# Performance work log

Measured on AMD Instinct MI355X. Metric: run time of the kernel, lower is better.

The kernel has to match this reference:

```python
import jax, jax.numpy as jnp
import numpy as np

DIM = 256
NH = 8
HGT = 32
WID = 32
B = 8


def rel_indices(S):
    # (1, S*S, S*S, 3) with channels (dx, dy, d^2), matching torch construction
    ind = jnp.arange(S)[None, :] - jnp.arange(S)[:, None]          # (S,S)
    indx = jnp.tile(ind, (S, S))                                    # (S^2,S^2)
    indy = jnp.repeat(jnp.repeat(ind, S, axis=0), S, axis=1)        # (S^2,S^2)
    indd = indx ** 2 + indy ** 2
    return jnp.stack([indx, indy, indd], axis=-1).astype(jnp.float32)[None]


def setup_inputs() -> dict:
    key = jax.random.key(0)
    ks = jax.random.split(key, 8)
    std = 0.02
    x = jax.random.normal(ks[0], (B, DIM, HGT, WID), dtype=jnp.float32)
    input_mask = jnp.ones((B, HGT, WID), dtype=jnp.float32)
    Wqk = jax.random.normal(ks[1], (2 * DIM, DIM), dtype=jnp.float32) * std  # qkv_bias=False
    Wv = jax.random.normal(ks[2], (DIM, DIM), dtype=jnp.float32) * std
    Wproj = jax.random.normal(ks[3], (DIM, DIM), dtype=jnp.float32) * std
    bproj = jnp.zeros((DIM,), dtype=jnp.float32)
    Wpos = jax.random.normal(ks[4], (NH, 3), dtype=jnp.float32) * std
    bpos = jnp.zeros((NH,), dtype=jnp.float32)
    gating = jnp.ones((NH,), dtype=jnp.float32)
    return {"x": x, "input_mask": input_mask, "Wqk": Wqk, "Wv": Wv,
            "Wproj": Wproj, "bproj": bproj, "Wpos": Wpos, "bpos": bpos,
            "gating": gating}


def gpsa_forward(x, input_mask, Wqk, Wv, Wproj, bproj, Wpos, bpos, gating):
    Bq, C, H, W = x.shape
    N = H * W
    nh = gating.shape[0]
    hd = C // nh
    scale = hd ** (-0.5)

    xf = x.reshape(Bq, C, N).transpose(0, 2, 1)          # (B,N,C)
    m = input_mask.reshape(Bq, N)                        # (B,N)

    qk = (xf @ Wqk.T).reshape(Bq, N, 2, nh, hd)
    q = qk[:, :, 0].transpose(0, 2, 1, 3)                # (B,nh,N,hd)
    k = qk[:, :, 1].transpose(0, 2, 1, 3)

    patch_score = jax.nn.softmax(
        jnp.einsum('bhnd,bhmd->bhnm', q, k) * scale, axis=-1)

    rel = rel_indices(H)                                  # (1,N,N,3)
    pos_score = jnp.einsum('unmt,ht->uhnm', rel, Wpos) + bpos[None, :, None, None]
    pos_score = jax.nn.softmax(pos_score, axis=-1)        # (1,nh,N,N)

    g = jax.nn.sigmoid(gating)[None, :, None, None]
    attn = (1.0 - g) * patch_score + g * pos_score
    attn = attn / attn.sum(axis=-1, keepdims=True)
    attn = attn * m[:, None, None, :]                     # mask keys
    attn = attn / attn.sum(axis=-1, keepdims=True)

    v = (xf @ Wv.T).reshape(Bq, N, nh, hd).transpose(0, 2, 1, 3)  # (B,nh,N,hd)
    out = jnp.einsum('bhnm,bhmd->bhnd', attn, v)          # (B,nh,N,hd)
    out = out.transpose(0, 2, 1, 3).reshape(Bq, N, C)
    out = out @ Wproj.T + bproj
    return out.transpose(0, 2, 1).reshape(Bq, C, H, W)


def reference(x, input_mask, Wqk, Wv, Wproj, bproj, Wpos, bpos, gating):
    return gpsa_forward(x, input_mask, Wqk, Wv, Wproj, bproj, Wpos, bpos, gating)
```

## Files before the change

kernel.cpp:

```cpp
#include <hip/hip_runtime.h>
#include <hip/hip_bf16.h>
#include <math.h>

#define B_ 8
#define C_ 256
#define N_ 1024
#define NH_ 8
#define HD_ 32

typedef __attribute__((ext_vector_type(8))) short bf16x8;
typedef __attribute__((ext_vector_type(4))) short bf16x4;
typedef __attribute__((ext_vector_type(4))) float f32x4;
typedef __attribute__((ext_vector_type(16))) float f32x16;
typedef __attribute__((ext_vector_type(2))) unsigned int u32x2;
typedef __attribute__((ext_vector_type(4))) unsigned int u32x4;
#define MFMA16(a,b,c) __builtin_amdgcn_mfma_f32_16x16x32_bf16((a),(b),(c),0,0,0)
#define MFMA32(a,b,c) __builtin_amdgcn_mfma_f32_32x32x16_bf16((a),(b),(c),0,0,0)

static __device__ __forceinline__ short f2bf(float f) {
    __hip_bfloat16 h = __float2bfloat16(f);
    return *reinterpret_cast<short*>(&h);
}
static __device__ __forceinline__ unsigned int cvtpk(float a, float b) {
    unsigned int r;
    asm("v_cvt_pk_bf16_f32 %0, %1, %2" : "=v"(r) : "v"(a), "v"(b));
    return r;
}

#define FS 0.2550352584f

static constexpr size_t OFF_VB   = 0;
static constexpr size_t OFF_QBF  = 8388608;
static constexpr size_t OFF_KFR  = 12582912;
static constexpr size_t OFF_VFR  = 16777216;
static constexpr size_t OFF_E1   = 20971520;
static constexpr size_t OFF_E2   = 21004288;
static constexpr size_t OFF_SE1  = 21037056;
static constexpr size_t OFF_SE2  = 21038080;
static constexpr size_t OFF_A2   = 21039104;
static constexpr size_t A2S      = 36;
static constexpr size_t OFF_O    = 30476288;
static constexpr size_t OFF_WBF  = 34670592;
static constexpr size_t OFF_WPBF = 35063808;
static constexpr size_t OFF_ZFR  = 35194880;

__global__ __launch_bounds__(256) void k_prep(
    const float* __restrict__ Wqk, const float* __restrict__ Wv,
    const float* __restrict__ Wp, const float* __restrict__ mask,
    const float* __restrict__ Wpos, const float* __restrict__ bpos,
    __hip_bfloat16* __restrict__ wfm, __hip_bfloat16* __restrict__ wpfm,
    __hip_bfloat16* __restrict__ zfrag,
    float* __restrict__ e1, float* __restrict__ e2,
    float* __restrict__ se1, float* __restrict__ se2)
{
    const int bx = blockIdx.x;
    const int tid = threadIdx.x;
    __shared__ float ps[2][32][8];
    if (bx < 256) {
        int idx = bx * 256 + tid;
        int row = idx >> 6;
        int c4  = (idx & 63) * 4;
        const float* src = (row < 512) ? (Wqk + (size_t)row*256)
                         : (row < 768) ? (Wv + (size_t)(row-512)*256)
                                       : (Wp + (size_t)(row-768)*256);
        float4 v = *(const float4*)(src + c4);
        bf16x4 pk;
        pk[0] = f2bf(v.x); pk[1] = f2bf(v.y); pk[2] = f2bf(v.z); pk[3] = f2bf(v.w);
        int r2 = (row < 768) ? row : (row - 768);
        __hip_bfloat16* dst = (row < 768) ? wfm : wpfm;
        size_t addr = (size_t)(r2 >> 4)*4096 + (size_t)(c4 >> 5)*512
                    + (size_t)((((c4 >> 3) & 3)*16) + (r2 & 15))*8 + (c4 & 7);
        *(bf16x4*)(dst + addr) = pk;
    } else if (bx < 384) {
        int idx = (bx - 256) * 256 + tid;
        int L8  = idx & 127;
        int mt  = (idx >> 7) & 31;
        int b   = idx >> 12;
        int region = L8 >> 6;
        int slot   = L8 & 63;
        int zrow = slot & 31, shi = slot >> 5;
        bf16x8 v;
        if (zrow == 0) {
            int m = mt*32 + region*16 + shi*8;
            const float* mp = mask + (size_t)b*N_ + m;
            #pragma unroll
            for (int j = 0; j < 8; ++j) v[j] = f2bf(mp[j]);
        } else {
            short c = (zrow == 1) ? (short)0x3F80 : (short)0;
            #pragma unroll
            for (int j = 0; j < 8; ++j) v[j] = c;
        }
        *(bf16x8*)(zfrag + ((size_t)b*32 + mt)*1024 + region*512 + slot*8) = v;
    } else {
        const int h = bx - 384;
        const int i = tid >> 3, j4 = (tid & 7) * 4;
        const float wx = Wpos[h*3+0], wy = Wpos[h*3+1], wd = Wpos[h*3+2], bp = bpos[h];
        float fmx = -1e30f, gmx = -1e30f;
        for (int jp = 0; jp < 32; ++jp) {
            float dx = (float)(jp - i);
            float q2 = wd*dx*dx;
            fmx = fmaxf(fmx, wx*dx + q2 + bp);
            gmx = fmaxf(gmx, wy*dx + q2);
        }
        float s1 = 0.f, s2 = 0.f;
        #pragma unroll
        for (int jj = 0; jj < 4; ++jj) {
            int j = j4 + jj;
            float dx = (float)(j - i);
            float q2 = wd*dx*dx;
            float fv = __expf(wx*dx + q2 + bp - fmx);
            float gv = __expf(wy*dx + q2 - gmx);
            e1[h*1024 + i*32 + j] = fv;
            e2[h*1024 + i*32 + j] = gv;
            s1 += fv; s2 += gv;
        }
        ps[0][i][tid & 7] = s1;
        ps[1][i][tid & 7] = s2;
        __syncthreads();
        if (tid < 32) {
            float a = 0.f, c = 0.f;
            #pragma unroll
            for (int k = 0; k < 8; ++k) { a += ps[0][tid][k]; c += ps[1][tid][k]; }
            se1[h*32 + tid] = a;
            se2[h*32 + tid] = c;
        }
    }
}

__global__ __launch_bounds__(256) void k_xT(
    const float* __restrict__ x, __hip_bfloat16* __restrict__ xfm)
{
    const int n0 = blockIdx.x * 64, c0 = blockIdx.y * 64, b = blockIdx.z;
    __shared__ float tile[64][68];
    const int t = threadIdx.x;
    {
        int cl = t >> 2, nq = (t & 3) * 16;
        const float* src = x + ((size_t)b*C_ + c0 + cl)*N_ + n0 + nq;
        #pragma unroll
        for (int i = 0; i < 4; ++i)
            *(float4*)&tile[cl][nq + i*4] = ((const float4*)src)[i];
    }
    __syncthreads();
    {
        int nl = t >> 2, cq = (t & 3) * 16;
        short pk[16];
        #pragma unroll
        for (int i = 0; i < 16; ++i) pk[i] = f2bf(tile[cq + i][nl]);
        int cg = c0 + cq;
        int ks = cg >> 5, g0 = (cg >> 3) & 3;
        size_t base = ((size_t)b*64 + (n0 >> 4) + (nl >> 4))*4096
                    + (size_t)ks*512 + (size_t)(g0*16 + (nl & 15))*8;
        *(uint4*)(xfm + base)       = *(uint4*)&pk[0];
        *(uint4*)(xfm + base + 128) = *(uint4*)&pk[8];
    }
}

__global__ __launch_bounds__(256) void k_qkv_mfma(
    const __hip_bfloat16* __restrict__ xfm, const __hip_bfloat16* __restrict__ wfm,
    const float* __restrict__ mask,
    __hip_bfloat16* __restrict__ qbf, __hip_bfloat16* __restrict__ kfrag,
    __hip_bfloat16* __restrict__ vfrag, float* __restrict__ vbuf)
{
    const int t = threadIdx.x, w = t >> 6, L = t & 63, lo = L & 15, g = L >> 4;
    const int jw = blockIdx.x * 64 + w * 16;
    const int n0 = blockIdx.y * 64, b = blockIdx.z;

    const __hip_bfloat16* afm = wfm + (size_t)(jw >> 4)*4096 + (size_t)L*8;
    bf16x8 af[8];
    #pragma unroll
    for (int ks = 0; ks < 8; ++ks) af[ks] = *(const bf16x8*)(afm + ks*512);

    const f32x4 Z = {0.f,0.f,0.f,0.f};
    f32x4 D0 = Z, D1 = Z, D2 = Z, D3 = Z;
    const __hip_bfloat16* xb = xfm + ((size_t)b*64 + (n0 >> 4))*4096 + (size_t)L*8;
    #pragma unroll
    for (int ks = 0; ks < 8; ++ks) {
        bf16x8 b0 = *(const bf16x8*)(xb + ks*512);
        bf16x8 b1 = *(const bf16x8*)(xb + 4096 + ks*512);
        bf16x8 b2 = *(const bf16x8*)(xb + 8192 + ks*512);
        bf16x8 b3 = *(const bf16x8*)(xb + 12288 + ks*512);
        D0 = MFMA16(af[ks], b0, D0);
        D1 = MFMA16(af[ks], b1, D1);
        D2 = MFMA16(af[ks], b2, D2);
        D3 = MFMA16(af[ks], b3, D3);
    }
    f32x4 D[4] = {D0, D1, D2, D3};

    const size_t bb = (size_t)b*NH_;
    if (jw < 256) {
        int h = jw >> 5, d0 = (jw & 31) + 4*g;
        #pragma unroll
        for (int nt = 0; nt < 4; ++nt) {
            int nn = n0 + nt*16 + lo;
            bf16x4 pk;
            #pragma unroll
            for (int r = 0; r < 4; ++r) pk[r] = f2bf(D[nt][r] * FS);
            *(bf16x4*)(qbf + ((bb + h)*N_ + nn)*HD_ + d0) = pk;
        }
    } else if (jw < 512) {
        int j2 = jw & 255, h = j2 >> 5, d0 = (j2 & 31) + 4*g;
        size_t base = (bb + h)*32768 + (size_t)(d0 >> 4)*512
                    + (size_t)((d0 >> 3) & 1)*256 + (d0 & 7);
        #pragma unroll
        for (int nt = 0; nt < 4; ++nt) {
            int nn = n0 + nt*16 + lo;
            bf16x4 pk;
            #pragma unroll
            for (int r = 0; r < 4; ++r) pk[r] = f2bf(D[nt][r]);
            *(bf16x4*)(kfrag + base + (size_t)(nn >> 5)*1024 + (nn & 31)*8) = pk;
        }
    } else {
        int j2 = jw - 512, h = j2 >> 5, d0 = (j2 & 31) + 4*g;
        #pragma unroll
        for (int nt = 0; nt < 4; ++nt) {
            int nn = n0 + nt*16 + lo;
            float mval = mask[(size_t)b*N_ + nn];
            float4 fv = make_float4(D[nt][0], D[nt][1], D[nt][2], D[nt][3]);
            *(float4*)(vbuf + ((bb + h)*N_ + nn)*HD_ + d0) = fv;
            size_t vbase = (bb + h)*32768 + (size_t)(nn >> 5)*1024
                         + (size_t)((nn >> 4) & 1)*512 + (size_t)((nn >> 3) & 1)*256
                         + (nn & 7);
            #pragma unroll
            for (int r = 0; r < 4; ++r)
                vfrag[vbase + (size_t)(d0 + r)*8] = __float2bfloat16(D[nt][r] * mval);
        }
    }
}

__global__ __launch_bounds__(256) void k_pos_apply(
    const float* __restrict__ vb, const float* __restrict__ mask,
    const float* __restrict__ e1, const float* __restrict__ e2,
    float* __restrict__ a2)
{
    const int rn = blockIdx.x, h = blockIdx.y, b = blockIdx.z;
    const int tid = threadIdx.x;
    const int cm = tid >> 3, dq = tid & 7;
    __shared__ float t1[32][36];
    __shared__ float e1s[32][36];
    __shared__ float t1m[32];
    __shared__ float e2s[32];
    const float* vbh = vb + (((size_t)b*NH_ + h)*N_)*HD_;
    const float* mb  = mask + (size_t)b*N_;

    {
        int r = tid >> 3, c4 = (tid & 7) * 4;
        *(float4*)&e1s[r][c4] = *(const float4*)(e1 + h*1024 + r*32 + c4);
        if (tid < 32) e2s[tid] = e2[h*1024 + rn*32 + tid];
    }
    __syncthreads();

    {
        float4 acc = make_float4(0.f,0.f,0.f,0.f);
        const float* vcol = vbh + cm*HD_ + dq*4;
        #pragma unroll 8
        for (int rm = 0; rm < 32; ++rm) {
            float4 vv = *(const float4*)(vcol + (size_t)rm*32*HD_);
            float wgt = e2s[rm];
            acc.x = fmaf(wgt, vv.x, acc.x);
            acc.y = fmaf(wgt, vv.y, acc.y);
            acc.z = fmaf(wgt, vv.z, acc.z);
            acc.w = fmaf(wgt, vv.w, acc.w);
        }
        *(float4*)&t1[cm][dq*4] = acc;
    }
    if (tid < 32) {
        float s = 0.f;
        for (int rm = 0; rm < 32; ++rm)
            s = fmaf(e2s[rm], mb[rm*32 + tid], s);
        t1m[tid] = s;
    }
    __syncthreads();

    const size_t bh = (size_t)b*NH_ + h;
    {
        const int cn = cm;
        float4 acc = make_float4(0.f,0.f,0.f,0.f);
        #pragma unroll 8
        for (int ci = 0; ci < 32; ++ci) {
            float wgt = e1s[cn][ci];
            float4 tv = *(const float4*)&t1[ci][dq*4];
            acc.x = fmaf(wgt, tv.x, acc.x);
            acc.y = fmaf(wgt, tv.y, acc.y);
            acc.z = fmaf(wgt, tv.z, acc.z);
            acc.w = fmaf(wgt, tv.w, acc.w);
        }
        int n = rn*32 + cn;
        *(float4*)(a2 + (bh*N_ + n)*A2S + dq*4) = acc;
    }
    if (tid < 32) {
        float s = 0.f;
        for (int ci = 0; ci < 32; ++ci)
            s = fmaf(e1s[tid][ci], t1m[ci], s);
        a2[(bh*N_ + rn*32 + tid)*A2S + 32] = s;
    }
}

__global__ __launch_bounds__(512, 4) void k_attn_mfma(
    const __hip_bfloat16* __restrict__ qbf, const __hip_bfloat16* __restrict__ kfrag,
    const __hip_bfloat16* __restrict__ vfrag, const __hip_bfloat16* __restrict__ zfrag,
    const float* __restrict__ a2, const float* __restrict__ se1,
    const float* __restrict__ se2, const float* __restrict__ gating,
    __hip_bfloat16* __restrict__ ob)
{
    const int bid = blockIdx.x;
    const int swz = ((bid & 7) << 6) | (bid >> 3);
    const int xt = swz & 7, h = (swz >> 3) & 7, b = swz >> 6;

    const int t = threadIdx.x, w = t >> 6, L = t & 63;
    const int ln = L & 31, hi = L >> 5;
    const int nh = w & 3, sp = w >> 2;
    const int n0 = xt * 128 + nh * 32;
    const size_t bh = (size_t)b*NH_ + h;
    const __hip_bfloat16* qh = qbf + bh*(size_t)N_*HD_;
    const size_t spo = (size_t)sp * 16 * 1024;
    const __hip_bfloat16* kf = kfrag + bh*32768 + spo + (size_t)L*8;
    const __hip_bfloat16* vf = vfrag + bh*32768 + spo + (size_t)L*8;
    const __hip_bfloat16* zf = zfrag + (size_t)b*32768 + spo + (size_t)L*8;

    __shared__ float ldsO[128*32];
    __shared__ float ldsZ[128*2];

    bf16x8 qf0 = *(const bf16x8*)(qh + (size_t)(n0 + ln)*HD_ + 8*hi);
    bf16x8 qf1 = *(const bf16x8*)(qh + (size_t)(n0 + ln)*HD_ + 16 + 8*hi);

    f32x16 O; f32x16 Zc;
    #pragma unroll
    for (int i = 0; i < 16; ++i) { O[i] = 0.f; Zc[i] = 0.f; }

    bf16x8 ka0 = *(const bf16x8*)(kf);
    bf16x8 ka1 = *(const bf16x8*)(kf + 512);
    bf16x8 vf0 = *(const bf16x8*)(vf);
    bf16x8 vf1 = *(const bf16x8*)(vf + 512);
    bf16x8 zf0 = *(const bf16x8*)(zf);
    bf16x8 zf1 = *(const bf16x8*)(zf + 512);

    for (int mt = 0; mt < 16; ++mt) {
        f32x16 S;
        #pragma unroll
        for (int i = 0; i < 16; ++i) S[i] = 0.f;
        S = MFMA32(ka0, qf0, S);
        S = MFMA32(ka1, qf1, S);

        const size_t o1 = (size_t)(mt < 15 ? mt + 1 : mt) * 1024;
        bf16x8 nka0 = *(const bf16x8*)(kf + o1);
        bf16x8 nka1 = *(const bf16x8*)(kf + o1 + 512);
        bf16x8 nvf0 = *(const bf16x8*)(vf + o1);
        bf16x8 nvf1 = *(const bf16x8*)(vf + o1 + 512);
        bf16x8 nzf0 = *(const bf16x8*)(zf + o1);
        bf16x8 nzf1 = *(const bf16x8*)(zf + o1 + 512);

        float e[16];
        #pragma unroll
        for (int i = 0; i < 16; ++i) e[i] = exp2f(S[i]);

        unsigned int x01 = cvtpk(e[0], e[1]), x23 = cvtpk(e[2], e[3]);
        unsigned int x45 = cvtpk(e[4], e[5]), x67 = cvtpk(e[6], e[7]);
        u32x2 r02 = __builtin_amdgcn_permlane32_swap(x01, x45, false, false);
        u32x2 r13 = __builtin_amdgcn_permlane32_swap(x23, x67, false, false);
        u32x4 p0u = { r02[0], r13[0], r02[1], r13[1] };
        bf16x8 pa0 = *reinterpret_cast<bf16x8*>(&p0u);
        unsigned int y01 = cvtpk(e[8], e[9]),  y23 = cvtpk(e[10], e[11]);
        unsigned int y45 = cvtpk(e[12], e[13]), y67 = cvtpk(e[14], e[15]);
        u32x2 s02 = __builtin_amdgcn_permlane32_swap(y01, y45, false, false);
        u32x2 s13 = __builtin_amdgcn_permlane32_swap(y23, y67, false, false);
        u32x4 p1u = { s02[0], s13[0], s02[1], s13[1] };
        bf16x8 pa1 = *reinterpret_cast<bf16x8*>(&p1u);

        O  = MFMA32(pa0, vf0, O);
        O  = MFMA32(pa1, vf1, O);
        Zc = MFMA32(pa0, zf0, Zc);
        Zc = MFMA32(pa1, zf1, Zc);

        ka0 = nka0; ka1 = nka1; vf0 = nvf0; vf1 = nvf1; zf0 = nzf0; zf1 = nzf1;
    }

    if (sp == 1) {
        #pragma unroll
        for (int r = 0; r < 16; ++r) {
            int nl = nh*32 + (r&3) + 8*(r>>2) + 4*hi;
            ldsO[nl*32 + ln] = O[r];
        }
        if (ln < 2) {
            #pragma unroll
            for (int r = 0; r < 16; ++r) {
                int nl = nh*32 + (r&3) + 8*(r>>2) + 4*hi;
                ldsZ[nl*2 + ln] = Zc[r];
            }
        }
    }
    __syncthreads();
    if (sp == 0) {
        #pragma unroll
        for (int r = 0; r < 16; ++r) {
            int nl = nh*32 + (r&3) + 8*(r>>2) + 4*hi;
            O[r] += ldsO[nl*32 + ln];
            if (ln < 2) Zc[r] += ldsZ[nl*2 + ln];
        }

        const float gs = 1.f / (1.f + __expf(-gating[h]));
        #pragma unroll
        for (int r = 0; r < 16; ++r) {
            const int n = n0 + (r&3) + 8*(r>>2) + 4*hi;
            float z1m = __shfl(Zc[r], (L & 32) | 0);
            float zsv = __shfl(Zc[r], (L & 32) | 1);
            const float* a2p = a2 + (bh*N_ + n)*A2S;
            float z2m = a2p[32];
            float zp  = se1[h*32 + (n & 31)] * se2[h*32 + (n >> 5)];
            float w1  = (1.f - gs) / zsv;
            float w2  = gs / zp;
            float inv = 1.f / (w1*z1m + w2*z2m);
            float o = (w1*O[r] + w2*a2p[ln]) * inv;
            ob[((size_t)b*N_ + n)*C_ + h*HD_ + ln] = __float2bfloat16(o);
        }
    }
}

__global__ __launch_bounds__(256) void k_proj_mfma(
    const __hip_bfloat16* __restrict__ obf, const __hip_bfloat16* __restrict__ wpfm,
    const float* __restrict__ bp, float* __restrict__ out)
{
    const int t = threadIdx.x, w = t >> 6, L = t & 63, lo = L & 15, g = L >> 4;
    const int cw = blockIdx.x * 64 + w * 16;
    const int n0 = blockIdx.y * 64, b = blockIdx.z;

    const __hip_bfloat16* afm = wpfm + (size_t)(cw >> 4)*4096 + (size_t)L*8;
    bf16x8 af[8];
    #pragma unroll
    for (int ks = 0; ks < 8; ++ks) af[ks] = *(const bf16x8*)(afm + ks*512);

    const f32x4 Z = {0.f,0.f,0.f,0.f};
    f32x4 D0 = Z, D1 = Z, D2 = Z, D3 = Z;
    const __hip_bfloat16* xb = obf + ((size_t)b*N_ + n0 + lo)*256 + 8*g;
    #pragma unroll
    for (int ks = 0; ks < 8; ++ks) {
        bf16x8 b0 = *(const bf16x8*)(xb + ks*32);
        bf16x8 b1 = *(const bf16x8*)(xb + 16*256 + ks*32);
        bf16x8 b2 = *(const bf16x8*)(xb + 32*256 + ks*32);
        bf16x8 b3 = *(const bf16x8*)(xb + 48*256 + ks*32);
        D0 = MFMA16(af[ks], b0, D0);
        D1 = MFMA16(af[ks], b1, D1);
        D2 = MFMA16(af[ks], b2, D2);
        D3 = MFMA16(af[ks], b3, D3);
    }
    f32x4 D[4] = {D0, D1, D2, D3};

    float bias[4];
    #pragma unroll
    for (int r = 0; r < 4; ++r) bias[r] = bp[cw + 4*g + r];
    #pragma unroll
    for (int nt = 0; nt < 4; ++nt) {
        int nn = n0 + nt*16 + lo;
        #pragma unroll
        for (int r = 0; r < 4; ++r)
            out[((size_t)b*C_ + cw + 4*g + r)*N_ + nn] = D[nt][r] + bias[r];
    }
}

extern "C" void kernel_launch(void* const* d_in, const int* in_sizes, int n_in,
                              void* d_out, int out_size, void* d_ws, size_t ws_size,
                              hipStream_t stream)
{
    (void)in_sizes; (void)n_in; (void)out_size; (void)ws_size;
    const float* x      = (const float*)d_in[0];
    const float* mask   = (const float*)d_in[1];
    const float* Wqk    = (const float*)d_in[2];
    const float* Wv     = (const float*)d_in[3];
    const float* Wproj  = (const float*)d_in[4];
    const float* bproj  = (const float*)d_in[5];
    const float* Wpos   = (const float*)d_in[6];
    const float* bpos   = (const float*)d_in[7];
    const float* gating = (const float*)d_in[8];
    float* out = (float*)d_out;
    char* w = (char*)d_ws;

    float*          vbuf  = (float*)(w + OFF_VB);
    __hip_bfloat16* qbf   = (__hip_bfloat16*)(w + OFF_QBF);
    __hip_bfloat16* kfrag = (__hip_bfloat16*)(w + OFF_KFR);
    __hip_bfloat16* vfrag = (__hip_bfloat16*)(w + OFF_VFR);
    float*          e1    = (float*)(w + OFF_E1);
    float*          e2    = (float*)(w + OFF_E2);
    float*          se1   = (float*)(w + OFF_SE1);
    float*          se2   = (float*)(w + OFF_SE2);
    float*          a2    = (float*)(w + OFF_A2);
    __hip_bfloat16* obf   = (__hip_bfloat16*)(w + OFF_O);
    __hip_bfloat16* xfm   = (__hip_bfloat16*)(w + OFF_O);
    __hip_bfloat16* wfm   = (__hip_bfloat16*)(w + OFF_WBF);
    __hip_bfloat16* wpfm  = (__hip_bfloat16*)(w + OFF_WPBF);
    __hip_bfloat16* zfrag = (__hip_bfloat16*)(w + OFF_ZFR);

    k_prep<<<dim3(392), dim3(256), 0, stream>>>(Wqk, Wv, Wproj, mask, Wpos, bpos,
                                                wfm, wpfm, zfrag, e1, e2, se1, se2);
    k_xT<<<dim3(16,4,8), dim3(256), 0, stream>>>(x, xfm);
    k_qkv_mfma<<<dim3(12,16,8), dim3(256), 0, stream>>>(xfm, wfm, mask, qbf, kfrag, vfrag, vbuf);
    k_pos_apply<<<dim3(32,8,8), dim3(256), 0, stream>>>(vbuf, mask, e1, e2, a2);
    k_attn_mfma<<<dim3(512), dim3(512), 0, stream>>>(qbf, kfrag, vfrag, zfrag, a2, se1, se2, gating, obf);
    k_proj_mfma<<<dim3(4,16,8), dim3(256), 0, stream>>>(obf, wpfm, bproj, out);
}
```

Before: 84.47 us.

## Merge x transpose into prep kernel and store attention output in MFMA fragment layout

The separate x-transpose kernel is folded into k_prep as extra blocks, which removes one launch and lets the transpose run concurrently with the weight and mask prep blocks. Separately, the attention kernel now writes its bf16 output directly in the fragment-major layout that the projection kernel reads, so each lane's B-operand load becomes contiguous. The cost is that every k_prep block now reserves the 17KB transpose tile in shared memory, which may lower occupancy for the other prep branches. The attention output stores also become more scattered.

```diff
diff --git a/kernel.cpp b/kernel.cpp
--- a/kernel.cpp
+++ b/kernel.cpp
@@ -48,14 +48,16 @@
     const float* __restrict__ Wqk, const float* __restrict__ Wv,
     const float* __restrict__ Wp, const float* __restrict__ mask,
     const float* __restrict__ Wpos, const float* __restrict__ bpos,
+    const float* __restrict__ x,
     __hip_bfloat16* __restrict__ wfm, __hip_bfloat16* __restrict__ wpfm,
-    __hip_bfloat16* __restrict__ zfrag,
+    __hip_bfloat16* __restrict__ zfrag, __hip_bfloat16* __restrict__ xfm,
     float* __restrict__ e1, float* __restrict__ e2,
     float* __restrict__ se1, float* __restrict__ se2)
 {
     const int bx = blockIdx.x;
     const int tid = threadIdx.x;
     __shared__ float ps[2][32][8];
+    __shared__ float tile[64][68];
     if (bx < 256) {
         int idx = bx * 256 + tid;
         int row = idx >> 6;
@@ -91,7 +93,7 @@
             for (int j = 0; j < 8; ++j) v[j] = c;
         }
         *(bf16x8*)(zfrag + ((size_t)b*32 + mt)*1024 + region*512 + slot*8) = v;
-    } else {
+    } else if (bx < 392) {
         const int h = bx - 384;
         const int i = tid >> 3, j4 = (tid & 7) * 4;
         const float wx = Wpos[h*3+0], wy = Wpos[h*3+1], wd = Wpos[h*3+2], bp = bpos[h];
@@ -124,34 +126,29 @@
             se1[h*32 + tid] = a;
             se2[h*32 + tid] = c;
         }
-    }
-}
-
-__global__ __launch_bounds__(256) void k_xT(
-    const float* __restrict__ x, __hip_bfloat16* __restrict__ xfm)
-{
-    const int n0 = blockIdx.x * 64, c0 = blockIdx.y * 64, b = blockIdx.z;
-    __shared__ float tile[64][68];
-    const int t = threadIdx.x;
-    {
-        int cl = t >> 2, nq = (t & 3) * 16;
-        const float* src = x + ((size_t)b*C_ + c0 + cl)*N_ + n0 + nq;
-        #pragma unroll
-        for (int i = 0; i < 4; ++i)
-            *(float4*)&tile[cl][nq + i*4] = ((const float4*)src)[i];
-    }
-    __syncthreads();
-    {
-        int nl = t >> 2, cq = (t & 3) * 16;
-        short pk[16];
-        #pragma unroll
-        for (int i = 0; i < 16; ++i) pk[i] = f2bf(tile[cq + i][nl]);
-        int cg = c0 + cq;
-        int ks = cg >> 5, g0 = (cg >> 3) & 3;
-        size_t base = ((size_t)b*64 + (n0 >> 4) + (nl >> 4))*4096
-                    + (size_t)ks*512 + (size_t)(g0*16 + (nl & 15))*8;
-        *(uint4*)(xfm + base)       = *(uint4*)&pk[0];
-        *(uint4*)(xfm + base + 128) = *(uint4*)&pk[8];
+    } else {
+        const int bx2 = bx - 392;
+        const int n0 = (bx2 & 15) * 64, c0 = ((bx2 >> 4) & 3) * 64, b = bx2 >> 6;
+        {
+            int cl = tid >> 2, nq = (tid & 3) * 16;
+            const float* src = x + ((size_t)b*C_ + c0 + cl)*N_ + n0 + nq;
+            #pragma unroll
+            for (int i = 0; i < 4; ++i)
+                *(float4*)&tile[cl][nq + i*4] = ((const float4*)src)[i];
+        }
+        __syncthreads();
+        {
+            int nl = tid >> 2, cq = (tid & 3) * 16;
+            short pk[16];
+            #pragma unroll
+            for (int i = 0; i < 16; ++i) pk[i] = f2bf(tile[cq + i][nl]);
+            int cg = c0 + cq;
+            int ks = cg >> 5, g0 = (cg >> 3) & 3;
+            size_t base = ((size_t)b*64 + (n0 >> 4) + (nl >> 4))*4096
+                        + (size_t)ks*512 + (size_t)(g0*16 + (nl & 15))*8;
+            *(uint4*)(xfm + base)       = *(uint4*)&pk[0];
+            *(uint4*)(xfm + base + 128) = *(uint4*)&pk[8];
+        }
     }
 }
 
@@ -410,7 +407,9 @@
             float w2  = gs / zp;
             float inv = 1.f / (w1*z1m + w2*z2m);
             float o = (w1*O[r] + w2*a2p[ln]) * inv;
-            ob[((size_t)b*N_ + n)*C_ + h*HD_ + ln] = __float2bfloat16(o);
+            size_t oaddr = ((size_t)b*64 + (n >> 4))*4096 + (size_t)h*512
+                         + (size_t)((ln >> 3)*16 + (n & 15))*8 + (ln & 7);
+            ob[oaddr] = __float2bfloat16(o);
         }
     }
 }
@@ -430,13 +429,13 @@
 
     const f32x4 Z = {0.f,0.f,0.f,0.f};
     f32x4 D0 = Z, D1 = Z, D2 = Z, D3 = Z;
-    const __hip_bfloat16* xb = obf + ((size_t)b*N_ + n0 + lo)*256 + 8*g;
+    const __hip_bfloat16* xb = obf + ((size_t)b*64 + (n0 >> 4))*4096 + (size_t)L*8;
     #pragma unroll
     for (int ks = 0; ks < 8; ++ks) {
-        bf16x8 b0 = *(const bf16x8*)(xb + ks*32);
-        bf16x8 b1 = *(const bf16x8*)(xb + 16*256 + ks*32);
-        bf16x8 b2 = *(const bf16x8*)(xb + 32*256 + ks*32);
-        bf16x8 b3 = *(const bf16x8*)(xb + 48*256 + ks*32);
+        bf16x8 b0 = *(const bf16x8*)(xb + ks*512);
+        bf16x8 b1 = *(const bf16x8*)(xb + 4096 + ks*512);
+        bf16x8 b2 = *(const bf16x8*)(xb + 8192 + ks*512);
+        bf16x8 b3 = *(const bf16x8*)(xb + 12288 + ks*512);
         D0 = MFMA16(af[ks], b0, D0);
         D1 = MFMA16(af[ks], b1, D1);
         D2 = MFMA16(af[ks], b2, D2);
@@ -488,9 +487,8 @@
     __hip_bfloat16* wpfm  = (__hip_bfloat16*)(w + OFF_WPBF);
     __hip_bfloat16* zfrag = (__hip_bfloat16*)(w + OFF_ZFR);
 
-    k_prep<<<dim3(392), dim3(256), 0, stream>>>(Wqk, Wv, Wproj, mask, Wpos, bpos,
-                                                wfm, wpfm, zfrag, e1, e2, se1, se2);
-    k_xT<<<dim3(16,4,8), dim3(256), 0, stream>>>(x, xfm);
+    k_prep<<<dim3(904), dim3(256), 0, stream>>>(Wqk, Wv, Wproj, mask, Wpos, bpos, x,
+                                                wfm, wpfm, zfrag, xfm, e1, e2, se1, se2);
     k_qkv_mfma<<<dim3(12,16,8), dim3(256), 0, stream>>>(xfm, wfm, mask, qbf, kfrag, vfrag, vbuf);
     k_pos_apply<<<dim3(32,8,8), dim3(256), 0, stream>>>(vbuf, mask, e1, e2, a2);
     k_attn_mfma<<<dim3(512), dim3(512), 0, stream>>>(qbf, kfrag, vfrag, zfrag, a2, se1, se2, gating, obf);
```

Result: faster. 76.91 us (-8.9%).
